# Kernel tuning notes

Hardware: AMD Instinct MI355X
Metric: run time of the kernel (lower is better)

The kernel has to match this reference:

```python
import jax, jax.numpy as jnp
import numpy as np

N_USERS = 30000
N_ITEMS = 20000
EMBED = 64
N_UI_LAYERS = 2
MASK_RATE = 0.1
MODEL_CAT = 0.02
USER_CAT = 0.3
ITEM_CAT = 0.3
NNZ = 600000


def setup_inputs() -> dict:
    key = jax.random.key(0)
    ks = jax.random.split(key, 16)
    ui_rows = jax.random.randint(ks[0], (NNZ,), 0, N_USERS, dtype=jnp.int64 if jax.config.jax_enable_x64 else jnp.int32)
    ui_cols = jax.random.randint(ks[1], (NNZ,), 0, N_ITEMS, dtype=ui_rows.dtype)
    ui_vals = jax.random.uniform(ks[2], (NNZ,), dtype=jnp.float32) * 0.1
    image_feats = jax.random.normal(ks[3], (N_ITEMS, 4096), dtype=jnp.float32)
    text_feats = jax.random.normal(ks[4], (N_ITEMS, 768), dtype=jnp.float32)
    user_feats0 = jax.random.normal(ks[5], (N_USERS, 1536), dtype=jnp.float32)
    item_title = jax.random.normal(ks[6], (N_ITEMS, 1536), dtype=jnp.float32)
    W_img = jax.random.normal(ks[7], (EMBED, 4096), dtype=jnp.float32) * 0.02
    b_img = jnp.zeros((EMBED,), jnp.float32)
    W_txt = jax.random.normal(ks[8], (EMBED, 768), dtype=jnp.float32) * 0.02
    b_txt = jnp.zeros((EMBED,), jnp.float32)
    W_usr = jax.random.normal(ks[9], (EMBED, 1536), dtype=jnp.float32) * 0.02
    b_usr = jnp.zeros((EMBED,), jnp.float32)
    W_itm = jax.random.normal(ks[10], (EMBED, 1536), dtype=jnp.float32) * 0.02
    b_itm = jnp.zeros((EMBED,), jnp.float32)
    user_id_emb = jax.random.normal(ks[11], (N_USERS, EMBED), dtype=jnp.float32) * 0.02
    item_id_emb = jax.random.normal(ks[12], (N_ITEMS, EMBED), dtype=jnp.float32) * 0.02
    return dict(ui_rows=ui_rows, ui_cols=ui_cols, ui_vals=ui_vals,
                image_feats=image_feats, text_feats=text_feats,
                user_feats0=user_feats0, item_title=item_title,
                W_img=W_img, b_img=b_img, W_txt=W_txt, b_txt=b_txt,
                W_usr=W_usr, b_usr=b_usr, W_itm=W_itm, b_itm=b_itm,
                user_id_emb=user_id_emb, item_id_emb=item_id_emb)


def _l2n(x):
    # F.normalize(x, p=2, dim=1)
    n = jnp.sqrt(jnp.sum(x * x, axis=1, keepdims=True))
    return x / jnp.maximum(n, 1e-12)


def reference(ui_rows, ui_cols, ui_vals, image_feats, text_feats, user_feats0, item_title,
              W_img, b_img, W_txt, b_txt, W_usr, b_usr, W_itm, b_itm,
              user_id_emb, item_id_emb):
    # sparse.mm(ui_graph, x): gather item rows, scale by edge vals, scatter-add to users
    def spmm_ui(x):
        return jax.ops.segment_sum(ui_vals[:, None] * x[ui_cols], ui_rows, num_segments=N_USERS)

    def spmm_iu(x):  # transpose graph
        return jax.ops.segment_sum(ui_vals[:, None] * x[ui_rows], ui_cols, num_segments=N_ITEMS)

    # --- feature masking (randperm with fixed key) ---
    num_mask = int(MASK_RATE * N_ITEMS)
    perm = jax.random.permutation(jax.random.key(42), N_ITEMS)
    mask_nodes = perm[:num_mask]
    img_m = image_feats.at[mask_nodes].set(image_feats.mean(0))
    txt_m = text_feats.at[mask_nodes].set(text_feats.mean(0))
    itm_m = item_title.at[mask_nodes].set(item_title.mean(0))

    # --- dense projections (dropout p=0 -> identity) ---
    raw_image = image_feats @ W_img.T + b_img
    raw_text = text_feats @ W_txt.T + b_txt
    raw_item = item_title @ W_itm.T + b_itm
    img_e = img_m @ W_img.T + b_img
    txt_e = txt_m @ W_txt.T + b_txt
    usr_e = user_feats0 @ W_usr.T + b_usr
    itm_e = itm_m @ W_itm.T + b_itm

    # --- modality graph propagation (args.layers=1; torch loop recomputes from fixed feats) ---
    image_user = spmm_ui(img_e)
    image_item = spmm_iu(image_user)
    text_user = spmm_ui(txt_e)
    text_item = spmm_iu(text_user)

    user_feat_from_item = spmm_ui(itm_e)
    item_feats_out = spmm_iu(user_feat_from_item)
    item_prof = spmm_iu(usr_e)
    user_prof = spmm_ui(item_prof)

    # --- id-embedding LightGCN-ish propagation ---
    u = user_id_emb
    i = item_id_emb
    u_list = [u]
    i_list = [i]
    for l in range(N_UI_LAYERS):
        if l == N_UI_LAYERS - 1:
            u = jax.nn.softmax(spmm_ui(i), axis=-1)
            i = jax.nn.softmax(spmm_iu(u), axis=-1)
        else:
            u = spmm_ui(i)
            i = spmm_iu(u)
        u_list.append(u)
        i_list.append(i)
    u_g = jnp.mean(jnp.stack(u_list), axis=0)
    i_g = jnp.mean(jnp.stack(i_list), axis=0)

    u_g = u_g + MODEL_CAT * _l2n(image_user) + MODEL_CAT * _l2n(text_user)
    i_g = i_g + MODEL_CAT * _l2n(image_item) + MODEL_CAT * _l2n(text_item)
    u_g = u_g + USER_CAT * _l2n(user_prof)
    i_g = i_g + USER_CAT * _l2n(item_prof)
    u_g = u_g + ITEM_CAT * _l2n(user_feat_from_item)
    i_g = i_g + ITEM_CAT * _l2n(item_feats_out)

    return (u_g, i_g, image_item, text_item, image_user, text_user, usr_e, item_feats_out,
            user_prof, item_prof, user_feat_from_item, mask_nodes,
            raw_image, raw_text, raw_item)
```

## Files before the change

### kernel.cpp

```cpp
#include <hip/hip_runtime.h>
#include <hip/hip_bf16.h>
#include <cstdint>
#include <cstddef>

#define NU 30000
#define NI 20000
#define NMASK 2000
#define NBUCK 2048

static inline int cdiv(int a, int b){ return (a + b - 1) / b; }

typedef __attribute__((ext_vector_type(8))) short bf16x8;
typedef __attribute__((ext_vector_type(4))) float f32x4;

__device__ __forceinline__ uint32_t rotl32(uint32_t x, int r){ return (x<<r)|(x>>(32-r)); }

__device__ __forceinline__ void tf2x32(uint32_t k0, uint32_t k1,
                                       uint32_t x0, uint32_t x1,
                                       uint32_t& o0, uint32_t& o1)
{
  uint32_t k2 = k0 ^ k1 ^ 0x1BD11BDAu;
  x0 += k0; x1 += k1;
#define TFR(r) { x0 += x1; x1 = rotl32(x1,(r)); x1 ^= x0; }
  TFR(13) TFR(15) TFR(26) TFR(6)
  x0 += k1; x1 += k2 + 1u;
  TFR(17) TFR(29) TFR(16) TFR(24)
  x0 += k2; x1 += k0 + 2u;
  TFR(13) TFR(15) TFR(26) TFR(6)
  x0 += k0; x1 += k1 + 3u;
  TFR(17) TFR(29) TFR(16) TFR(24)
  x0 += k1; x1 += k2 + 4u;
  TFR(13) TFR(15) TFR(26) TFR(6)
  x0 += k2; x1 += k0 + 5u;
#undef TFR
  o0 = x0; o1 = x1;
}

__device__ __forceinline__ ushort f2bf(float f){
  __hip_bfloat16 h = __float2bfloat16(f);
  return *reinterpret_cast<ushort*>(&h);
}
__device__ __forceinline__ uint32_t pk2(float a, float b){
  __hip_bfloat162 h = __float22bfloat162_rn(make_float2(a, b));
  return *reinterpret_cast<uint32_t*>(&h);
}
__device__ __forceinline__ uint2 f4_to_bf4(float4 v){
  __hip_bfloat162 h0 = __float22bfloat162_rn(make_float2(v.x, v.y));
  __hip_bfloat162 h1 = __float22bfloat162_rn(make_float2(v.z, v.w));
  return make_uint2(*reinterpret_cast<uint32_t*>(&h0), *reinterpret_cast<uint32_t*>(&h1));
}
__device__ __forceinline__ float lobf(uint32_t p){
  union { uint32_t u; float f; } c; c.u = p << 16; return c.f;
}
__device__ __forceinline__ float hibf(uint32_t p){
  union { uint32_t u; float f; } c; c.u = p & 0xffff0000u; return c.f;
}
__device__ __forceinline__ float bf2f(ushort h){
  union { uint32_t u; float f; } c; c.u = (uint32_t)h << 16; return c.f;
}

#define WTOTAL (64*(4096+768+1536+1536))
__global__ __launch_bounds__(256) void prep_kernel(
    uint32_t* __restrict__ bits1, uint32_t* __restrict__ bits2,
    int* __restrict__ h1, int* __restrict__ h2,
    const float* __restrict__ wi, const float* __restrict__ wt,
    const float* __restrict__ wm, const float* __restrict__ wu,
    ushort* __restrict__ wbf)
{
  int i = blockIdx.x*256 + threadIdx.x;
  if (i < NI) {
    uint32_t c0,c1, s0,s1, t0,t1;
    tf2x32(0u,42u, 0u,0u, c0,c1);
    tf2x32(0u,42u, 0u,1u, s0,s1);
    tf2x32(c0,c1, 0u,1u, t0,t1);
    uint32_t o0,o1;
    tf2x32(s0,s1, 0u,(uint32_t)i, o0,o1);
    uint32_t b1 = o0^o1;
    tf2x32(t0,t1, 0u,(uint32_t)i, o0,o1);
    uint32_t b2 = o0^o1;
    bits1[i] = b1; bits2[i] = b2;
    atomicAdd(&h1[b1 >> 21], 1);
    atomicAdd(&h2[b2 >> 21], 1);
  }
  const int n0 = 64*4096, n1 = 64*768, n2 = 64*1536;
  for (int k = i; k < WTOTAL; k += gridDim.x*256) {
    float v;
    if (k < n0) v = wi[k];
    else if (k < n0+n1) v = wt[k-n0];
    else if (k < n0+n1+n2) v = wm[k-n0-n1];
    else v = wu[k-n0-n1-n2];
    wbf[k] = f2bf(v);
  }
}

__global__ __launch_bounds__(64) void exscan2_kernel(
    const int* __restrict__ h1, int* __restrict__ bb1,
    const int* __restrict__ h2, int* __restrict__ bb2)
{
  const int* cnt = blockIdx.x ? h2 : h1;
  int* ptr = blockIdx.x ? bb2 : bb1;
  int lane = threadIdx.x;
  int carry = 0;
  for (int base = 0; base < NBUCK; base += 64) {
    int i = base + lane;
    int v = cnt[i];
    int s = v;
#pragma unroll
    for (int off = 1; off < 64; off <<= 1) {
      int t = __shfl_up(s, off);
      if (lane >= off) s += t;
    }
    ptr[i] = carry + s - v;
    carry += __shfl(s, 63);
  }
  if (lane == 0) ptr[NBUCK] = carry;
}

__global__ __launch_bounds__(256) void scatter12_kernel(
    const uint32_t* __restrict__ bits1, const int* __restrict__ bb1, int* __restrict__ c1,
    uint64_t* __restrict__ barr1,
    const uint32_t* __restrict__ bits2, const int* __restrict__ bb2, int* __restrict__ c2,
    uint64_t* __restrict__ barr2, int n)
{
  int i = blockIdx.x*256 + threadIdx.x;
  if (i >= n) return;
  uint32_t k1 = bits1[i];
  int b = k1 >> 21;
  int p = bb1[b] + atomicAdd(&c1[b], 1);
  barr1[p] = ((uint64_t)k1 << 32) | (uint32_t)i;
  uint32_t k2 = bits2[i];
  b = k2 >> 21;
  p = bb2[b] + atomicAdd(&c2[b], 1);
  barr2[p] = ((uint64_t)k2 << 32) | (uint32_t)i;
}

template<int FINAL>
__global__ __launch_bounds__(256) void rank_bucket_kernel(
    const uint64_t* __restrict__ barr, const int* __restrict__ bptr,
    uint32_t* __restrict__ perm, float* __restrict__ mask_out, int* __restrict__ flag,
    int n)
{
  int p = blockIdx.x*256 + threadIdx.x;
  if (p >= n) return;
  uint64_t mk = barr[p];
  int b = (int)(mk >> 53);
  int p0 = bptr[b], p1 = bptr[b+1];
  int r = p0;
  for (int q = p0; q < p1; ++q) r += (int)(barr[q] < mk);
  uint32_t i = (uint32_t)mk;
  if (!FINAL) {
    perm[r] = i;
  } else if (r < NMASK) {
    uint32_t v = perm[i];
    mask_out[r] = (float)v;
    flag[v] = 1;
  }
}

__global__ __launch_bounds__(256) void gemm_mfma_kernel(
    const float* __restrict__ X, const ushort* __restrict__ Wbf,
    float* __restrict__ pbuf, int N, int K, int klen)
{
  __shared__ ushort Xs[64][72];
  __shared__ ushort Ws[64][72];
  const int tid = threadIdx.x;
  const int row0 = blockIdx.x * 64;
  const int kbeg = blockIdx.y * klen;
  const int lane = tid & 63;
  const int wr = tid >> 6;
  const int lrow = lane & 15;
  const int kslot = lane >> 4;
  f32x4 acc[4] = {f32x4{0,0,0,0},f32x4{0,0,0,0},f32x4{0,0,0,0},f32x4{0,0,0,0}};

  const int sr = tid >> 4;
  const int sc = (tid & 15) * 4;
  const int wrow = tid >> 2;
  const int wcol = (tid & 3) * 16;

  for (int k0 = kbeg; k0 < kbeg + klen; k0 += 64) {
#pragma unroll
    for (int i = 0; i < 4; ++i) {
      int r = sr + 16*i;
      int gr = row0 + r;
      float4 v = make_float4(0.f,0.f,0.f,0.f);
      if (gr < N) v = *reinterpret_cast<const float4*>(X + (size_t)gr*K + k0 + sc);
      *reinterpret_cast<uint2*>(&Xs[r][sc]) = f4_to_bf4(v);
    }
    {
      const ushort* wsrc = Wbf + (size_t)wrow*K + k0 + wcol;
      *reinterpret_cast<uint4*>(&Ws[wrow][wcol])   = *reinterpret_cast<const uint4*>(wsrc);
      *reinterpret_cast<uint4*>(&Ws[wrow][wcol+8]) = *reinterpret_cast<const uint4*>(wsrc + 8);
    }
    __syncthreads();
#pragma unroll
    for (int ks = 0; ks < 2; ++ks) {
      int kb = ks*32 + kslot*8;
      bf16x8 af = *reinterpret_cast<const bf16x8*>(&Xs[wr*16 + lrow][kb]);
#pragma unroll
      for (int ct = 0; ct < 4; ++ct) {
        bf16x8 bfr = *reinterpret_cast<const bf16x8*>(&Ws[ct*16 + lrow][kb]);
        acc[ct] = __builtin_amdgcn_mfma_f32_16x16x32_bf16(af, bfr, acc[ct], 0, 0, 0);
      }
    }
    __syncthreads();
  }
  float* pb = pbuf + (size_t)blockIdx.y * N * 64;
#pragma unroll
  for (int ct = 0; ct < 4; ++ct)
#pragma unroll
    for (int j = 0; j < 4; ++j) {
      int gr = row0 + wr*16 + kslot*4 + j;
      if (gr < N) pb[(size_t)gr*64 + ct*16 + lrow] = acc[ct][j];
    }
}

__global__ __launch_bounds__(256) void reduce4_kernel(
    const float* __restrict__ pb_img, const float* __restrict__ pb_txt,
    const float* __restrict__ pb_itm, const float* __restrict__ pb_usr,
    const float* __restrict__ b_img, const float* __restrict__ b_txt,
    const float* __restrict__ b_itm, const float* __restrict__ b_usr,
    const float* __restrict__ idemb,
    float* __restrict__ o_ri, float* __restrict__ o_rt, float* __restrict__ o_rit,
    float* __restrict__ o_ue, ushort* __restrict__ ue_bf,
    uint2* __restrict__ pk_all, float* __restrict__ means)
{
  __shared__ float red[3][256];
  const int nI = NI*64, nUx = NU*64;
  int lane = threadIdx.x & 63;
  int w = threadIdx.x >> 6;
  float sa = 0.f, sb = 0.f, sc = 0.f;
  for (int i = blockIdx.x*256 + threadIdx.x; i < nUx; i += gridDim.x*256) {
    int lc = i & 63;
    if (i < nI) {
      float s = b_img[lc];
#pragma unroll
      for (int c = 0; c < 8; ++c) s += pb_img[(size_t)c*nI + i];
      o_ri[i] = s;
      float t = b_txt[lc];
#pragma unroll
      for (int c = 0; c < 4; ++c) t += pb_txt[(size_t)c*nI + i];
      o_rt[i] = t;
      float u = b_itm[lc];
#pragma unroll
      for (int c = 0; c < 4; ++c) u += pb_itm[(size_t)c*nI + i];
      o_rit[i] = u;
      pk_all[i] = make_uint2(pk2(s, t), pk2(u, idemb[i]));
      sa += s; sb += t; sc += u;
    }
    float su = b_usr[lc];
#pragma unroll
    for (int c = 0; c < 6; ++c) su += pb_usr[(size_t)c*nUx + i];
    o_ue[i] = su; ue_bf[i] = f2bf(su);
  }
  red[0][threadIdx.x] = sa; red[1][threadIdx.x] = sb; red[2][threadIdx.x] = sc;
  __syncthreads();
  if (threadIdx.x < 64) {
#pragma unroll
    for (int q = 0; q < 3; ++q) {
      float t = red[q][lane]+red[q][64+lane]+red[q][128+lane]+red[q][192+lane];
      if (t != 0.f) atomicAdd(&means[q*64+lane], t * (1.f/NI));
    }
  }
}

__global__ __launch_bounds__(256) void hist_kernel(const int* __restrict__ rows,
                                                   const int* __restrict__ cols,
                                                   int* __restrict__ cu, int* __restrict__ ci, int nnz)
{
  int k = blockIdx.x*256 + threadIdx.x;
  if (k < nnz) { atomicAdd(&cu[rows[k]], 1); atomicAdd(&ci[cols[k]], 1); }
}

__global__ __launch_bounds__(256) void scan_block2_kernel(
    const int* __restrict__ cnt_u, const int* __restrict__ cnt_i,
    int* __restrict__ part_u, int* __restrict__ part_i,
    int* __restrict__ bsum_u, int* __restrict__ bsum_i, int nbu)
{
  __shared__ int wsum[4];
  bool isU = (int)blockIdx.x < nbu;
  int blk = isU ? blockIdx.x : blockIdx.x - nbu;
  const int* cnt = isU ? cnt_u : cnt_i;
  int* part = isU ? part_u : part_i;
  int* bsum = isU ? bsum_u : bsum_i;
  int n = isU ? NU : NI;
  int i = blk*256 + threadIdx.x;
  int lane = threadIdx.x & 63;
  int w = threadIdx.x >> 6;
  int v = (i < n) ? cnt[i] : 0;
  int s = v;
#pragma unroll
  for (int off = 1; off < 64; off <<= 1) {
    int t = __shfl_up(s, off);
    if (lane >= off) s += t;
  }
  if (lane == 63) wsum[w] = s;
  __syncthreads();
  int wo = 0;
#pragma unroll
  for (int k = 0; k < 4; ++k) if (k < w) wo += wsum[k];
  if (i < n) part[i] = wo + s - v;
  if (threadIdx.x == 255) bsum[blk] = wo + s;
}

__global__ __launch_bounds__(64) void exscan2b_kernel(
    const int* __restrict__ bs_u, int* __restrict__ bp_u, int nbu,
    const int* __restrict__ bs_i, int* __restrict__ bp_i, int nbi)
{
  const int* cnt = blockIdx.x ? bs_i : bs_u;
  int* ptr = blockIdx.x ? bp_i : bp_u;
  int n = blockIdx.x ? nbi : nbu;
  int lane = threadIdx.x;
  int carry = 0;
  for (int base = 0; base < n; base += 64) {
    int i = base + lane;
    int v = (i < n) ? cnt[i] : 0;
    int s = v;
#pragma unroll
    for (int off = 1; off < 64; off <<= 1) {
      int t = __shfl_up(s, off);
      if (lane >= off) s += t;
    }
    if (i < n) ptr[i] = carry + s - v;
    carry += __shfl(s, 63);
  }
  if (lane == 0) ptr[n] = carry;
}

__global__ __launch_bounds__(256) void scan_add2_kernel(
    const int* __restrict__ part_u, const int* __restrict__ bp_u,
    const int* __restrict__ part_i, const int* __restrict__ bp_i,
    int* __restrict__ ptr_u, int* __restrict__ cur_u,
    int* __restrict__ ptr_i, int* __restrict__ cur_i, int nbu, int nbi)
{
  bool isU = (int)blockIdx.x < nbu;
  int blk = isU ? blockIdx.x : blockIdx.x - nbu;
  int n = isU ? NU : NI;
  const int* part = isU ? part_u : part_i;
  const int* bp = isU ? bp_u : bp_i;
  int* ptr = isU ? ptr_u : ptr_i;
  int* cur = isU ? cur_u : cur_i;
  int i = blk*256 + threadIdx.x;
  if (i < n) { int v = part[i] + bp[blk]; ptr[i] = v; cur[i] = v; }
  if (i == 0) ptr[n] = bp[isU ? nbu : nbi];
}

__global__ __launch_bounds__(256) void scatter_kernel(
    const int* __restrict__ rows, const int* __restrict__ cols, const float* __restrict__ vals,
    int* __restrict__ cur_u, int* __restrict__ cur_i,
    int* __restrict__ idx_u, float* __restrict__ val_u,
    int* __restrict__ idx_i, float* __restrict__ val_i, int nnz)
{
  int k = blockIdx.x*256 + threadIdx.x;
  if (k < nnz) {
    int r = rows[k], c = cols[k];
    float v = vals[k];
    int pu = atomicAdd(&cur_u[r], 1);
    idx_u[pu] = c; val_u[pu] = v;
    int pi = atomicAdd(&cur_i[c], 1);
    idx_i[pi] = r; val_i[pi] = v;
  }
}

__global__ __launch_bounds__(256) void spmm_user1_kernel(
    const int* __restrict__ ptr, const int* __restrict__ idx, const float* __restrict__ val,
    const uint2* __restrict__ pka,
    const int* __restrict__ flag, const float* __restrict__ means,
    float* __restrict__ iu, float* __restrict__ tu, float* __restrict__ ufi, float* __restrict__ u1,
    uint2* __restrict__ qa, int nrows)
{
  int row = blockIdx.x*4 + (threadIdx.x >> 6);
  int lane = threadIdx.x & 63;
  if (row >= nrows) return;
  int p0 = ptr[row], p1 = ptr[row+1];
  float m0 = means[lane], m1 = means[64+lane], m2 = means[128+lane];
  float a0=0.f, a1=0.f, a2=0.f, a3=0.f;
#define U1STEP(gg,ff,ww) { float x0,x1,x2, x3 = hibf(gg.y); \
    if (ff) { x0=m0; x1=m1; x2=m2; } \
    else { x0=lobf(gg.x); x1=hibf(gg.x); x2=lobf(gg.y); } \
    a0=fmaf(ww,x0,a0); a1=fmaf(ww,x1,a1); a2=fmaf(ww,x2,a2); a3=fmaf(ww,x3,a3); }
  int p = p0;
  for (; p + 4 <= p1; p += 4) {
    int j0=idx[p+0], j1=idx[p+1], j2=idx[p+2], j3=idx[p+3];
    float w0=val[p+0], w1=val[p+1], w2=val[p+2], w3=val[p+3];
    int f0=flag[j0], f1=flag[j1], f2=flag[j2], f3=flag[j3];
    uint2 g0=pka[(size_t)j0*64+lane], g1=pka[(size_t)j1*64+lane];
    uint2 g2=pka[(size_t)j2*64+lane], g3=pka[(size_t)j3*64+lane];
    U1STEP(g0,f0,w0) U1STEP(g1,f1,w1) U1STEP(g2,f2,w2) U1STEP(g3,f3,w3)
  }
  for (; p < p1; ++p) {
    int j = idx[p]; float v = val[p];
    uint2 g = pka[(size_t)j*64 + lane];
    int f = flag[j];
    U1STEP(g,f,v)
  }
#undef U1STEP
  size_t o = (size_t)row*64 + lane;
  iu[o]=a0; tu[o]=a1; ufi[o]=a2; u1[o]=a3;
  qa[o] = make_uint2(pk2(a0, a1), pk2(a2, a3));
}

__global__ __launch_bounds__(256) void spmm_item1_kernel(
    const int* __restrict__ ptr, const int* __restrict__ idx, const float* __restrict__ val,
    const uint2* __restrict__ qa, const ushort* __restrict__ ueh,
    float* __restrict__ ii, float* __restrict__ ti, float* __restrict__ ifo,
    float* __restrict__ i1, float* __restrict__ ip,
    uint32_t* __restrict__ qip1, int nrows)
{
  int row = blockIdx.x*4 + (threadIdx.x >> 6);
  int lane = threadIdx.x & 63;
  if (row >= nrows) return;
  int p0 = ptr[row], p1 = ptr[row+1];
  float a0=0.f, a1=0.f, a2=0.f, a3=0.f, a4=0.f;
#define I1STEP(gg,uu,ww) { \
    a0=fmaf(ww,lobf(gg.x),a0); a1=fmaf(ww,hibf(gg.x),a1); \
    a2=fmaf(ww,lobf(gg.y),a2); a3=fmaf(ww,hibf(gg.y),a3); \
    a4=fmaf(ww,bf2f(uu),a4); }
  int p = p0;
  for (; p + 4 <= p1; p += 4) {
    int j0=idx[p+0], j1=idx[p+1], j2=idx[p+2], j3=idx[p+3];
    float w0=val[p+0], w1=val[p+1], w2=val[p+2], w3=val[p+3];
    size_t b0=(size_t)j0*64+lane, b1=(size_t)j1*64+lane, b2=(size_t)j2*64+lane, b3=(size_t)j3*64+lane;
    uint2 g0=qa[b0], g1=qa[b1], g2=qa[b2], g3=qa[b3];
    ushort u0=ueh[b0], u1_=ueh[b1], u2_=ueh[b2], u3_=ueh[b3];
    I1STEP(g0,u0,w0) I1STEP(g1,u1_,w1) I1STEP(g2,u2_,w2) I1STEP(g3,u3_,w3)
  }
  for (; p < p1; ++p) {
    int j = idx[p]; float v = val[p];
    size_t b = (size_t)j*64 + lane;
    uint2 g = qa[b]; ushort u = ueh[b];
    I1STEP(g,u,v)
  }
#undef I1STEP
  size_t o = (size_t)row*64 + lane;
  ii[o]=a0; ti[o]=a1; ifo[o]=a2; i1[o]=a3; ip[o]=a4;
  qip1[o] = pk2(a4, a3);
}

__global__ __launch_bounds__(256) void user2_kernel(
    const int* __restrict__ ptr, const int* __restrict__ idx, const float* __restrict__ val,
    const uint32_t* __restrict__ qip1,
    const float* __restrict__ idemb, const float* __restrict__ u1,
    const float* __restrict__ iu, const float* __restrict__ tu, const float* __restrict__ ufi,
    float* __restrict__ up, ushort* __restrict__ u2h, float* __restrict__ ug, int nrows)
{
  int row = blockIdx.x*4 + (threadIdx.x >> 6);
  int lane = threadIdx.x & 63;
  if (row >= nrows) return;
  int p0 = ptr[row], p1 = ptr[row+1];
  float aup=0.f, au2=0.f;
  int p = p0;
  for (; p + 4 <= p1; p += 4) {
    int j0=idx[p+0], j1=idx[p+1], j2=idx[p+2], j3=idx[p+3];
    float w0=val[p+0], w1=val[p+1], w2=val[p+2], w3=val[p+3];
    uint32_t g0=qip1[(size_t)j0*64+lane], g1=qip1[(size_t)j1*64+lane];
    uint32_t g2=qip1[(size_t)j2*64+lane], g3=qip1[(size_t)j3*64+lane];
    aup=fmaf(w0,lobf(g0),aup); au2=fmaf(w0,hibf(g0),au2);
    aup=fmaf(w1,lobf(g1),aup); au2=fmaf(w1,hibf(g1),au2);
    aup=fmaf(w2,lobf(g2),aup); au2=fmaf(w2,hibf(g2),au2);
    aup=fmaf(w3,lobf(g3),aup); au2=fmaf(w3,hibf(g3),au2);
  }
  for (; p < p1; ++p) {
    int j = idx[p]; float v = val[p];
    uint32_t g = qip1[(size_t)j*64 + lane];
    aup = fmaf(v, lobf(g), aup);
    au2 = fmaf(v, hibf(g), au2);
  }
  float m = au2;
#pragma unroll
  for (int o2=32;o2;o2>>=1) m = fmaxf(m, __shfl_xor(m, o2));
  float e = expf(au2 - m);
  float s = e;
#pragma unroll
  for (int o2=32;o2;o2>>=1) s += __shfl_xor(s, o2);
  float u2 = e / s;
  size_t o = (size_t)row*64 + lane;
  up[o] = aup; u2h[o] = f2bf(u2);
  float e0 = idemb[o], e1 = u1[o];
  float v1 = iu[o], v2 = tu[o], v3 = aup, v4 = ufi[o];
  float n1=v1*v1, n2=v2*v2, n3=v3*v3, n4=v4*v4;
#pragma unroll
  for (int o2=32;o2;o2>>=1) {
    n1 += __shfl_xor(n1, o2); n2 += __shfl_xor(n2, o2);
    n3 += __shfl_xor(n3, o2); n4 += __shfl_xor(n4, o2);
  }
  n1 = fmaxf(sqrtf(n1), 1e-12f); n2 = fmaxf(sqrtf(n2), 1e-12f);
  n3 = fmaxf(sqrtf(n3), 1e-12f); n4 = fmaxf(sqrtf(n4), 1e-12f);
  ug[o] = (e0+e1+u2)*(1.f/3.f)
        + 0.02f*(v1/n1) + 0.02f*(v2/n2)
        + 0.30f*(v3/n3) + 0.30f*(v4/n4);
}

__global__ __launch_bounds__(256) void item2_kernel(
    const int* __restrict__ ptr, const int* __restrict__ idx, const float* __restrict__ val,
    const ushort* __restrict__ u2h,
    const float* __restrict__ idemb, const float* __restrict__ i1,
    const float* __restrict__ ii, const float* __restrict__ ti,
    const float* __restrict__ ip, const float* __restrict__ ifo,
    float* __restrict__ ig, int nrows)
{
  int row = blockIdx.x*4 + (threadIdx.x >> 6);
  int lane = threadIdx.x & 63;
  if (row >= nrows) return;
  int p0 = ptr[row], p1 = ptr[row+1];
  float ai2=0.f;
  int p = p0;
  for (; p + 4 <= p1; p += 4) {
    int j0=idx[p+0], j1=idx[p+1], j2=idx[p+2], j3=idx[p+3];
    float w0=val[p+0], w1=val[p+1], w2=val[p+2], w3=val[p+3];
    ushort h0=u2h[(size_t)j0*64+lane], h1=u2h[(size_t)j1*64+lane];
    ushort h2=u2h[(size_t)j2*64+lane], h3=u2h[(size_t)j3*64+lane];
    ai2=fmaf(w0,bf2f(h0),ai2); ai2=fmaf(w1,bf2f(h1),ai2);
    ai2=fmaf(w2,bf2f(h2),ai2); ai2=fmaf(w3,bf2f(h3),ai2);
  }
  for (; p < p1; ++p) {
    int j = idx[p]; float v = val[p];
    ai2 = fmaf(v, bf2f(u2h[(size_t)j*64 + lane]), ai2);
  }
  float m = ai2;
#pragma unroll
  for (int o2=32;o2;o2>>=1) m = fmaxf(m, __shfl_xor(m, o2));
  float e = expf(ai2 - m);
  float s = e;
#pragma unroll
  for (int o2=32;o2;o2>>=1) s += __shfl_xor(s, o2);
  float i2 = e / s;
  size_t o = (size_t)row*64 + lane;
  float e0 = idemb[o], e1 = i1[o];
  float v1 = ii[o], v2 = ti[o], v3 = ip[o], v4 = ifo[o];
  float n1=v1*v1, n2=v2*v2, n3=v3*v3, n4=v4*v4;
#pragma unroll
  for (int o2=32;o2;o2>>=1) {
    n1 += __shfl_xor(n1, o2); n2 += __shfl_xor(n2, o2);
    n3 += __shfl_xor(n3, o2); n4 += __shfl_xor(n4, o2);
  }
  n1 = fmaxf(sqrtf(n1), 1e-12f); n2 = fmaxf(sqrtf(n2), 1e-12f);
  n3 = fmaxf(sqrtf(n3), 1e-12f); n4 = fmaxf(sqrtf(n4), 1e-12f);
  ig[o] = (e0+e1+i2)*(1.f/3.f)
        + 0.02f*(v1/n1) + 0.02f*(v2/n2)
        + 0.30f*(v3/n3) + 0.30f*(v4/n4);
}

extern "C" void kernel_launch(void* const* d_in, const int* in_sizes, int n_in,
                              void* d_out, int out_size, void* d_ws, size_t ws_size,
                              hipStream_t stream)
{
  const int*   ui_rows     = (const int*)d_in[0];
  const int*   ui_cols     = (const int*)d_in[1];
  const float* ui_vals     = (const float*)d_in[2];
  const float* image_feats = (const float*)d_in[3];
  const float* text_feats  = (const float*)d_in[4];
  const float* user_feats0 = (const float*)d_in[5];
  const float* item_title  = (const float*)d_in[6];
  const float* W_img = (const float*)d_in[7];
  const float* b_img = (const float*)d_in[8];
  const float* W_txt = (const float*)d_in[9];
  const float* b_txt = (const float*)d_in[10];
  const float* W_usr = (const float*)d_in[11];
  const float* b_usr = (const float*)d_in[12];
  const float* W_itm = (const float*)d_in[13];
  const float* b_itm = (const float*)d_in[14];
  const float* user_id_emb = (const float*)d_in[15];
  const float* item_id_emb = (const float*)d_in[16];
  const int nnz = in_sizes[0];

  float* out = (float*)d_out;
  const size_t OU = (size_t)NU*64, OI = (size_t)NI*64;
  size_t off = 0;
  float* o_ug   = out + off; off += OU;
  float* o_ig   = out + off; off += OI;
  float* o_ii   = out + off; off += OI;
  float* o_ti   = out + off; off += OI;
  float* o_iu   = out + off; off += OU;
  float* o_tu   = out + off; off += OU;
  float* o_ue   = out + off; off += OU;
  float* o_ifo  = out + off; off += OI;
  float* o_up   = out + off; off += OU;
  float* o_ip   = out + off; off += OI;
  float* o_ufi  = out + off; off += OU;
  float* o_mask = out + off; off += NMASK;
  float* o_ri   = out + off; off += OI;
  float* o_rt   = out + off; off += OI;
  float* o_rit  = out + off; off += OI;

  char* wp = (char*)d_ws;
  auto walloc = [&](size_t bytes) -> char* {
    char* r = wp; wp += (bytes + 255) & ~(size_t)255; return r;
  };
  int*   cnt_u = (int*)  walloc((size_t)NU*4);
  int*   cnt_i = (int*)  walloc((size_t)NI*4);
  int*   flag  = (int*)  walloc((size_t)NI*4);
  float* means = (float*)walloc(3*64*4);
  int*   h1    = (int*)  walloc(NBUCK*4);
  int*   c1    = (int*)  walloc(NBUCK*4);
  int*   h2    = (int*)  walloc(NBUCK*4);
  int*   c2    = (int*)  walloc(NBUCK*4);
  size_t zero_bytes = (size_t)(wp - (char*)d_ws);
  uint32_t* bits1 = (uint32_t*)walloc((size_t)NI*4);
  uint32_t* bits2 = (uint32_t*)walloc((size_t)NI*4);
  uint32_t* permA = (uint32_t*)walloc((size_t)NI*4);
  uint64_t* barr1 = (uint64_t*)walloc((size_t)NI*8);
  uint64_t* barr2 = (uint64_t*)walloc((size_t)NI*8);
  int*   bb1   = (int*)  walloc((NBUCK+1)*4);
  int*   bb2   = (int*)  walloc((NBUCK+1)*4);
  int*   ptr_u = (int*)  walloc((size_t)(NU+1)*4);
  int*   ptr_i = (int*)  walloc((size_t)(NI+1)*4);
  int*   cur_u = (int*)  walloc((size_t)NU*4);
  int*   cur_i = (int*)  walloc((size_t)NI*4);
  int*   idx_u = (int*)  walloc((size_t)nnz*4);
  float* val_u = (float*)walloc((size_t)nnz*4);
  int*   idx_i = (int*)  walloc((size_t)nnz*4);
  float* val_i = (float*)walloc((size_t)nnz*4);
  float* u1    = (float*)walloc(OU*4);
  float* i1    = (float*)walloc(OI*4);
  int*   part_u = (int*) walloc((size_t)NU*4);
  int*   part_i = (int*) walloc((size_t)NI*4);
  int*   bsum_u = (int*) walloc(128*4);
  int*   bsum_i = (int*) walloc(128*4);
  int*   bp_u   = (int*) walloc(129*4);
  int*   bp_i   = (int*) walloc(129*4);
  ushort* wbf  = (ushort*)walloc((size_t)WTOTAL*2);
  uint2* pk_all = (uint2*)walloc(OI*8);
  uint2* q_all  = (uint2*)walloc(OU*8);
  uint32_t* qip1 = (uint32_t*)walloc(OI*4);
  ushort*   ue_bf = (ushort*)walloc(OU*2);
  ushort*   u2h   = (ushort*)walloc(OU*2);
  float* pb_img = (float*)walloc((size_t)8*NI*64*4);
  float* pb_txt = (float*)walloc((size_t)4*NI*64*4);
  float* pb_itm = (float*)walloc((size_t)4*NI*64*4);
  float* pb_usr = (float*)walloc((size_t)6*NU*64*4);
  ushort* wbf_img = wbf;
  ushort* wbf_txt = wbf + 64*4096;
  ushort* wbf_itm = wbf_txt + 64*768;
  ushort* wbf_usr = wbf_itm + 64*1536;

  hipMemsetAsync(d_ws, 0, zero_bytes, stream);

  const int GB = cdiv(NI,256);
  prep_kernel<<<512, 256, 0, stream>>>(bits1, bits2, h1, h2, W_img, W_txt, W_itm, W_usr, wbf);
  exscan2_kernel<<<2, 64, 0, stream>>>(h1, bb1, h2, bb2);
  scatter12_kernel<<<GB, 256, 0, stream>>>(bits1, bb1, c1, barr1, bits2, bb2, c2, barr2, NI);
  rank_bucket_kernel<0><<<GB, 256, 0, stream>>>(barr1, bb1, permA, nullptr, nullptr, NI);
  rank_bucket_kernel<1><<<GB, 256, 0, stream>>>(barr2, bb2, permA, o_mask, flag, NI);

  {
    dim3 g1(cdiv(NI,64), 8);
    gemm_mfma_kernel<<<g1, 256, 0, stream>>>(image_feats, wbf_img, pb_img, NI, 4096, 512);
    dim3 g2(cdiv(NI,64), 4);
    gemm_mfma_kernel<<<g2, 256, 0, stream>>>(text_feats,  wbf_txt, pb_txt, NI, 768, 192);
    dim3 g3(cdiv(NI,64), 4);
    gemm_mfma_kernel<<<g3, 256, 0, stream>>>(item_title,  wbf_itm, pb_itm, NI, 1536, 384);
    dim3 g4(cdiv(NU,64), 6);
    gemm_mfma_kernel<<<g4, 256, 0, stream>>>(user_feats0, wbf_usr, pb_usr, NU, 1536, 256);
  }
  reduce4_kernel<<<512, 256, 0, stream>>>(pb_img, pb_txt, pb_itm, pb_usr,
      b_img, b_txt, b_itm, b_usr, item_id_emb,
      o_ri, o_rt, o_rit, o_ue, ue_bf, pk_all, means);

  hist_kernel<<<cdiv(nnz,256), 256, 0, stream>>>(ui_rows, ui_cols, cnt_u, cnt_i, nnz);
  {
    int nbu = cdiv(NU,256), nbi = cdiv(NI,256);
    scan_block2_kernel<<<nbu+nbi, 256, 0, stream>>>(cnt_u, cnt_i, part_u, part_i, bsum_u, bsum_i, nbu);
    exscan2b_kernel<<<2, 64, 0, stream>>>(bsum_u, bp_u, nbu, bsum_i, bp_i, nbi);
    scan_add2_kernel<<<nbu+nbi, 256, 0, stream>>>(part_u, bp_u, part_i, bp_i,
        ptr_u, cur_u, ptr_i, cur_i, nbu, nbi);
  }
  scatter_kernel<<<cdiv(nnz,256), 256, 0, stream>>>(ui_rows, ui_cols, ui_vals,
      cur_u, cur_i, idx_u, val_u, idx_i, val_i, nnz);

  const int GU = cdiv(NU,4), GI = cdiv(NI,4);
  spmm_user1_kernel<<<GU,256,0,stream>>>(ptr_u, idx_u, val_u,
      pk_all, flag, means,
      o_iu, o_tu, o_ufi, u1, q_all, NU);
  spmm_item1_kernel<<<GI,256,0,stream>>>(ptr_i, idx_i, val_i,
      q_all, ue_bf,
      o_ii, o_ti, o_ifo, i1, o_ip, qip1, NI);
  user2_kernel<<<GU,256,0,stream>>>(ptr_u, idx_u, val_u,
      qip1, user_id_emb, u1, o_iu, o_tu, o_ufi,
      o_up, u2h, o_ug, NU);
  item2_kernel<<<GI,256,0,stream>>>(ptr_i, idx_i, val_i,
      u2h, item_id_emb, i1, o_ii, o_ti, o_ip, o_ifo,
      o_ig, NI);
}
```

Baseline: 578.1 us.

## Merge GEMM launches, store bf16 partials, fold histogram into prep, deepen SpMM unroll

Replaces the four per-matrix GEMM launches with one flat-grid kernel that dispatches blocks to each projection, so the small GEMMs can run concurrently with the large image one. Split-K partial sums are now written and read back as bf16 instead of fp32, halving that traffic at some accuracy cost. The edge-count histogram moves into the prep kernel, removing a launch. The first-layer SpMM kernels gain an 8-way unrolled gather loop to keep more loads in flight, and the reduce launch grows to 1024 blocks.

```diff
diff --git a/kernel.cpp b/kernel.cpp
--- a/kernel.cpp
+++ b/kernel.cpp
@@ -65,7 +65,9 @@
     int* __restrict__ h1, int* __restrict__ h2,
     const float* __restrict__ wi, const float* __restrict__ wt,
     const float* __restrict__ wm, const float* __restrict__ wu,
-    ushort* __restrict__ wbf)
+    ushort* __restrict__ wbf,
+    const int* __restrict__ rows, const int* __restrict__ cols,
+    int* __restrict__ cnt_u, int* __restrict__ cnt_i, int nnz)
 {
   int i = blockIdx.x*256 + threadIdx.x;
   if (i < NI) {
@@ -91,6 +93,10 @@
     else v = wu[k-n0-n1-n2];
     wbf[k] = f2bf(v);
   }
+  for (int k = i; k < nnz; k += gridDim.x*256) {
+    atomicAdd(&cnt_u[rows[k]], 1);
+    atomicAdd(&cnt_i[cols[k]], 1);
+  }
 }
 
 __global__ __launch_bounds__(64) void exscan2_kernel(
@@ -157,15 +163,39 @@
   }
 }
 
-__global__ __launch_bounds__(256) void gemm_mfma_kernel(
-    const float* __restrict__ X, const ushort* __restrict__ Wbf,
-    float* __restrict__ pbuf, int N, int K, int klen)
+#define RB_I 313
+#define RB_U 469
+__global__ __launch_bounds__(256) void gemm_all_kernel(
+    const float* __restrict__ Xi, const float* __restrict__ Xt,
+    const float* __restrict__ Xm, const float* __restrict__ Xu,
+    const ushort* __restrict__ wbf,
+    ushort* __restrict__ pb_img, ushort* __restrict__ pb_txt,
+    ushort* __restrict__ pb_itm, ushort* __restrict__ pb_usr)
 {
   __shared__ ushort Xs[64][72];
   __shared__ ushort Ws[64][72];
+  const int bid = blockIdx.x;
+  const float* X; const ushort* Wbf; ushort* pb;
+  int N, K, klen, rb, ch;
+  if (bid < RB_I*8) {
+    X = Xi; Wbf = wbf; pb = pb_img; N = NI; K = 4096; klen = 512;
+    rb = bid % RB_I; ch = bid / RB_I;
+  } else if (bid < RB_I*12) {
+    int l = bid - RB_I*8;
+    X = Xt; Wbf = wbf + 64*4096; pb = pb_txt; N = NI; K = 768; klen = 192;
+    rb = l % RB_I; ch = l / RB_I;
+  } else if (bid < RB_I*16) {
+    int l = bid - RB_I*12;
+    X = Xm; Wbf = wbf + 64*(4096+768); pb = pb_itm; N = NI; K = 1536; klen = 384;
+    rb = l % RB_I; ch = l / RB_I;
+  } else {
+    int l = bid - RB_I*16;
+    X = Xu; Wbf = wbf + 64*(4096+768+1536); pb = pb_usr; N = NU; K = 1536; klen = 256;
+    rb = l % RB_U; ch = l / RB_U;
+  }
   const int tid = threadIdx.x;
-  const int row0 = blockIdx.x * 64;
-  const int kbeg = blockIdx.y * klen;
+  const int row0 = rb * 64;
+  const int kbeg = ch * klen;
   const int lane = tid & 63;
   const int wr = tid >> 6;
   const int lrow = lane & 15;
@@ -204,19 +234,19 @@
     }
     __syncthreads();
   }
-  float* pb = pbuf + (size_t)blockIdx.y * N * 64;
+  ushort* pbc = pb + (size_t)ch * N * 64;
 #pragma unroll
   for (int ct = 0; ct < 4; ++ct)
 #pragma unroll
     for (int j = 0; j < 4; ++j) {
       int gr = row0 + wr*16 + kslot*4 + j;
-      if (gr < N) pb[(size_t)gr*64 + ct*16 + lrow] = acc[ct][j];
+      if (gr < N) pbc[(size_t)gr*64 + ct*16 + lrow] = f2bf(acc[ct][j]);
     }
 }
 
 __global__ __launch_bounds__(256) void reduce4_kernel(
-    const float* __restrict__ pb_img, const float* __restrict__ pb_txt,
-    const float* __restrict__ pb_itm, const float* __restrict__ pb_usr,
+    const ushort* __restrict__ pb_img, const ushort* __restrict__ pb_txt,
+    const ushort* __restrict__ pb_itm, const ushort* __restrict__ pb_usr,
     const float* __restrict__ b_img, const float* __restrict__ b_txt,
     const float* __restrict__ b_itm, const float* __restrict__ b_usr,
     const float* __restrict__ idemb,
@@ -227,29 +257,28 @@
   __shared__ float red[3][256];
   const int nI = NI*64, nUx = NU*64;
   int lane = threadIdx.x & 63;
-  int w = threadIdx.x >> 6;
   float sa = 0.f, sb = 0.f, sc = 0.f;
   for (int i = blockIdx.x*256 + threadIdx.x; i < nUx; i += gridDim.x*256) {
     int lc = i & 63;
     if (i < nI) {
       float s = b_img[lc];
 #pragma unroll
-      for (int c = 0; c < 8; ++c) s += pb_img[(size_t)c*nI + i];
+      for (int c = 0; c < 8; ++c) s += bf2f(pb_img[(size_t)c*nI + i]);
       o_ri[i] = s;
       float t = b_txt[lc];
 #pragma unroll
-      for (int c = 0; c < 4; ++c) t += pb_txt[(size_t)c*nI + i];
+      for (int c = 0; c < 4; ++c) t += bf2f(pb_txt[(size_t)c*nI + i]);
       o_rt[i] = t;
       float u = b_itm[lc];
 #pragma unroll
-      for (int c = 0; c < 4; ++c) u += pb_itm[(size_t)c*nI + i];
+      for (int c = 0; c < 4; ++c) u += bf2f(pb_itm[(size_t)c*nI + i]);
       o_rit[i] = u;
       pk_all[i] = make_uint2(pk2(s, t), pk2(u, idemb[i]));
       sa += s; sb += t; sc += u;
     }
     float su = b_usr[lc];
 #pragma unroll
-    for (int c = 0; c < 6; ++c) su += pb_usr[(size_t)c*nUx + i];
+    for (int c = 0; c < 6; ++c) su += bf2f(pb_usr[(size_t)c*nUx + i]);
     o_ue[i] = su; ue_bf[i] = f2bf(su);
   }
   red[0][threadIdx.x] = sa; red[1][threadIdx.x] = sb; red[2][threadIdx.x] = sc;
@@ -261,14 +290,6 @@
       if (t != 0.f) atomicAdd(&means[q*64+lane], t * (1.f/NI));
     }
   }
-}
-
-__global__ __launch_bounds__(256) void hist_kernel(const int* __restrict__ rows,
-                                                   const int* __restrict__ cols,
-                                                   int* __restrict__ cu, int* __restrict__ ci, int nnz)
-{
-  int k = blockIdx.x*256 + threadIdx.x;
-  if (k < nnz) { atomicAdd(&cu[rows[k]], 1); atomicAdd(&ci[cols[k]], 1); }
 }
 
 __global__ __launch_bounds__(256) void scan_block2_kernel(
@@ -379,6 +400,15 @@
     else { x0=lobf(gg.x); x1=hibf(gg.x); x2=lobf(gg.y); } \
     a0=fmaf(ww,x0,a0); a1=fmaf(ww,x1,a1); a2=fmaf(ww,x2,a2); a3=fmaf(ww,x3,a3); }
   int p = p0;
+  for (; p + 8 <= p1; p += 8) {
+    int j[8]; float w[8]; int f[8]; uint2 g[8];
+#pragma unroll
+    for (int q = 0; q < 8; ++q) { j[q]=idx[p+q]; w[q]=val[p+q]; }
+#pragma unroll
+    for (int q = 0; q < 8; ++q) { f[q]=flag[j[q]]; g[q]=pka[(size_t)j[q]*64+lane]; }
+#pragma unroll
+    for (int q = 0; q < 8; ++q) U1STEP(g[q],f[q],w[q])
+  }
   for (; p + 4 <= p1; p += 4) {
     int j0=idx[p+0], j1=idx[p+1], j2=idx[p+2], j3=idx[p+3];
     float w0=val[p+0], w1=val[p+1], w2=val[p+2], w3=val[p+3];
@@ -416,6 +446,18 @@
     a2=fmaf(ww,lobf(gg.y),a2); a3=fmaf(ww,hibf(gg.y),a3); \
     a4=fmaf(ww,bf2f(uu),a4); }
   int p = p0;
+  for (; p + 8 <= p1; p += 8) {
+    int j[8]; float w[8]; uint2 g[8]; ushort u[8];
+#pragma unroll
+    for (int q = 0; q < 8; ++q) { j[q]=idx[p+q]; w[q]=val[p+q]; }
+#pragma unroll
+    for (int q = 0; q < 8; ++q) {
+      size_t b = (size_t)j[q]*64+lane;
+      g[q]=qa[b]; u[q]=ueh[b];
+    }
+#pragma unroll
+    for (int q = 0; q < 8; ++q) I1STEP(g[q],u[q],w[q])
+  }
   for (; p + 4 <= p1; p += 4) {
     int j0=idx[p+0], j1=idx[p+1], j2=idx[p+2], j3=idx[p+3];
     float w0=val[p+0], w1=val[p+1], w2=val[p+2], w3=val[p+3];
@@ -624,39 +666,29 @@
   uint32_t* qip1 = (uint32_t*)walloc(OI*4);
   ushort*   ue_bf = (ushort*)walloc(OU*2);
   ushort*   u2h   = (ushort*)walloc(OU*2);
-  float* pb_img = (float*)walloc((size_t)8*NI*64*4);
-  float* pb_txt = (float*)walloc((size_t)4*NI*64*4);
-  float* pb_itm = (float*)walloc((size_t)4*NI*64*4);
-  float* pb_usr = (float*)walloc((size_t)6*NU*64*4);
-  ushort* wbf_img = wbf;
-  ushort* wbf_txt = wbf + 64*4096;
-  ushort* wbf_itm = wbf_txt + 64*768;
-  ushort* wbf_usr = wbf_itm + 64*1536;
+  ushort* pb_img = (ushort*)walloc((size_t)8*NI*64*2);
+  ushort* pb_txt = (ushort*)walloc((size_t)4*NI*64*2);
+  ushort* pb_itm = (ushort*)walloc((size_t)4*NI*64*2);
+  ushort* pb_usr = (ushort*)walloc((size_t)6*NU*64*2);
 
   hipMemsetAsync(d_ws, 0, zero_bytes, stream);
 
+  prep_kernel<<<512, 256, 0, stream>>>(bits1, bits2, h1, h2,
+      W_img, W_txt, W_itm, W_usr, wbf, ui_rows, ui_cols, cnt_u, cnt_i, nnz);
+
   const int GB = cdiv(NI,256);
-  prep_kernel<<<512, 256, 0, stream>>>(bits1, bits2, h1, h2, W_img, W_txt, W_itm, W_usr, wbf);
   exscan2_kernel<<<2, 64, 0, stream>>>(h1, bb1, h2, bb2);
   scatter12_kernel<<<GB, 256, 0, stream>>>(bits1, bb1, c1, barr1, bits2, bb2, c2, barr2, NI);
   rank_bucket_kernel<0><<<GB, 256, 0, stream>>>(barr1, bb1, permA, nullptr, nullptr, NI);
   rank_bucket_kernel<1><<<GB, 256, 0, stream>>>(barr2, bb2, permA, o_mask, flag, NI);
 
-  {
-    dim3 g1(cdiv(NI,64), 8);
-    gemm_mfma_kernel<<<g1, 256, 0, stream>>>(image_feats, wbf_img, pb_img, NI, 4096, 512);
-    dim3 g2(cdiv(NI,64), 4);
-    gemm_mfma_kernel<<<g2, 256, 0, stream>>>(text_feats,  wbf_txt, pb_txt, NI, 768, 192);
-    dim3 g3(cdiv(NI,64), 4);
-    gemm_mfma_kernel<<<g3, 256, 0, stream>>>(item_title,  wbf_itm, pb_itm, NI, 1536, 384);
-    dim3 g4(cdiv(NU,64), 6);
-    gemm_mfma_kernel<<<g4, 256, 0, stream>>>(user_feats0, wbf_usr, pb_usr, NU, 1536, 256);
-  }
-  reduce4_kernel<<<512, 256, 0, stream>>>(pb_img, pb_txt, pb_itm, pb_usr,
+  gemm_all_kernel<<<RB_I*16 + RB_U*6, 256, 0, stream>>>(
+      image_feats, text_feats, item_title, user_feats0, wbf,
+      pb_img, pb_txt, pb_itm, pb_usr);
+  reduce4_kernel<<<1024, 256, 0, stream>>>(pb_img, pb_txt, pb_itm, pb_usr,
       b_img, b_txt, b_itm, b_usr, item_id_emb,
       o_ri, o_rt, o_rit, o_ue, ue_bf, pk_all, means);
 
-  hist_kernel<<<cdiv(nnz,256), 256, 0, stream>>>(ui_rows, ui_cols, cnt_u, cnt_i, nnz);
   {
     int nbu = cdiv(NU,256), nbi = cdiv(NI,256);
     scan_block2_kernel<<<nbu+nbi, 256, 0, stream>>>(cnt_u, cnt_i, part_u, part_i, bsum_u, bsum_i, nbu);
```

Measured after the change: 540.1 us. -6.6%, faster.
